# Kernel optimization log

Hardware: AMD Instinct MI355X
Metric: run time of the kernel (lower is better)

The kernel has to match this reference:

```python
import jax, jax.numpy as jnp
import numpy as np

EMBED_DIM = 32
HIDDEN_DIM = 16

def _xavier(key, fan_in, fan_out):
    limit = float(np.sqrt(6.0 / (fan_in + fan_out)))
    return jax.random.uniform(key, (fan_in, fan_out), jnp.float32, -limit, limit)

def setup_inputs() -> dict:
    key = jax.random.key(0)
    ks = jax.random.split(key, 7)
    N = 1_000_000
    H = jax.random.normal(ks[0], (N, EMBED_DIM), jnp.float32)
    TPL = jax.random.normal(ks[1], (1, 1), jnp.float32)
    # params (xavier-uniform weights, zero biases, matching torch init)
    Wv = _xavier(ks[2], EMBED_DIM, HIDDEN_DIM); bv = jnp.zeros((HIDDEN_DIM,), jnp.float32)
    Wu = _xavier(ks[3], EMBED_DIM, HIDDEN_DIM); bu = jnp.zeros((HIDDEN_DIM,), jnp.float32)
    Ww = _xavier(ks[4], HIDDEN_DIM, 1);        bw = jnp.zeros((1,), jnp.float32)
    W1 = _xavier(ks[5], EMBED_DIM + 1, HIDDEN_DIM); b1 = jnp.zeros((HIDDEN_DIM,), jnp.float32)
    W2 = _xavier(ks[6], HIDDEN_DIM, 1);        b2 = jnp.zeros((1,), jnp.float32)
    return {"H": H, "TPL": TPL, "Wv": Wv, "bv": bv, "Wu": Wu, "bu": bu,
            "Ww": Ww, "bw": bw, "W1": W1, "b1": b1, "W2": W2, "b2": b2}

def reference(H, TPL, Wv, bv, Wu, bu, Ww, bw, W1, b1, W2, b2):
    # Gated attention: V (tanh branch) * U (sigmoid branch); dropout off (eval mode)
    V = jnp.tanh(H @ Wv + bv)                       # (N, hid)
    U = jax.nn.sigmoid(H @ Wu + bu)                 # (N, hid)
    G = V * U                                       # (N, hid)
    A_raw = G @ Ww + bw                             # (N, 1)
    alpha = jax.nn.softmax(A_raw.T, axis=1)         # (1, N)
    B = alpha @ H                                   # (1, D) attention-pooled bag rep
    B_fused = jnp.concatenate([B, TPL], axis=1)     # (1, D+1)
    h = jax.nn.relu(B_fused @ W1 + b1)              # (1, hid)
    score = h @ W2 + b2                             # (1, 1)
    return (score, alpha)
```

## Files before the change

kernel.cpp:

```cpp
#include <hip/hip_runtime.h>

#define NBLK   1024
#define TPB    256
#define D      32
#define HID    16
#define CHUNK  16
#define STRIDE 36
#define NWAVES (NBLK * 4)

__global__ __launch_bounds__(TPB, 4)
void k1_logits(const float* __restrict__ H,
               const float* __restrict__ Wv, const float* __restrict__ bv,
               const float* __restrict__ Wu, const float* __restrict__ bu,
               const float* __restrict__ Ww, const float* __restrict__ bw,
               float* __restrict__ eout,
               float* __restrict__ partials,
               int N)
{
    __shared__ float lds[TPB / 64][CHUNK * STRIDE];
    __shared__ float red[TPB / 64][D + 1];

    const int tid  = threadIdx.x;
    const int wave = tid >> 6;
    const int lane = tid & 63;
    const int g    = lane >> 4;
    const int h    = lane & 15;

    float wv[D], wu[D];
    #pragma unroll
    for (int d = 0; d < D; ++d) {
        wv[d] = Wv[d * HID + h];
        wu[d] = Wu[d * HID + h];
    }
    const float bvh = bv[h], buh = bu[h], wwh = Ww[h], bw0 = bw[0];

    float s_acc = 0.0f, vec0 = 0.0f, vec1 = 0.0f;

    float* slice = lds[wave];
    const int nchunk = N / CHUNK;
    int c = blockIdx.x * (TPB / 64) + wave;

    float4 pre0, pre1;
    bool has = (c < nchunk);
    if (has) {
        const float4* src = reinterpret_cast<const float4*>(H + (size_t)c * CHUNK * D);
        pre0 = src[lane];
        pre1 = src[lane + 64];
    }

    while (has) {
        const int cn = c + NWAVES;
        const bool hn = (cn < nchunk);
        float4 nxt0, nxt1;
        if (hn) {
            const float4* src = reinterpret_cast<const float4*>(H + (size_t)cn * CHUNK * D);
            nxt0 = src[lane];
            nxt1 = src[lane + 64];
        }

        {
            const int f0 = lane,      r0i = f0 >> 3, q0 = f0 & 7;
            const int f1 = lane + 64, r1i = f1 >> 3, q1 = f1 & 7;
            *reinterpret_cast<float4*>(&slice[r0i * STRIDE + q0 * 4]) = pre0;
            *reinterpret_cast<float4*>(&slice[r1i * STRIDE + q1 * 4]) = pre1;
        }

        float my_e = 0.0f;
        #pragma unroll
        for (int s = 0; s < 4; ++s) {
            const int rr = s * 4 + g;
            const float* row = &slice[rr * STRIDE];

            float v = bvh, u = buh;
            #pragma unroll
            for (int q = 0; q < 8; ++q) {
                const float4 t4 = *reinterpret_cast<const float4*>(&row[q * 4]);
                v = fmaf(t4.x, wv[q * 4 + 0], v);  u = fmaf(t4.x, wu[q * 4 + 0], u);
                v = fmaf(t4.y, wv[q * 4 + 1], v);  u = fmaf(t4.y, wu[q * 4 + 1], u);
                v = fmaf(t4.z, wv[q * 4 + 2], v);  u = fmaf(t4.z, wu[q * 4 + 2], u);
                v = fmaf(t4.w, wv[q * 4 + 3], v);  u = fmaf(t4.w, wu[q * 4 + 3], u);
            }
            const float th = 1.0f - 2.0f / (__expf(2.0f * v) + 1.0f);
            const float sg = 1.0f / (1.0f + __expf(-u));
            float pa = th * sg * wwh;
            pa += __shfl_xor(pa, 1);
            pa += __shfl_xor(pa, 2);
            pa += __shfl_xor(pa, 4);
            pa += __shfl_xor(pa, 8);
            const float e = __expf(pa + bw0);
            if (h == s) my_e = e;
            s_acc += e;
            const float2 rp = *reinterpret_cast<const float2*>(&row[2 * h]);
            vec0 = fmaf(e, rp.x, vec0);
            vec1 = fmaf(e, rp.y, vec1);
        }
        if (h < 4) eout[c * CHUNK + h * 4 + g] = my_e;

        pre0 = nxt0; pre1 = nxt1;
        c = cn;
        has = hn;
    }

    s_acc += __shfl_xor(s_acc, 16);  s_acc += __shfl_xor(s_acc, 32);
    vec0  += __shfl_xor(vec0, 16);   vec0  += __shfl_xor(vec0, 32);
    vec1  += __shfl_xor(vec1, 16);   vec1  += __shfl_xor(vec1, 32);

    if (lane == 0) red[wave][0] = s_acc;
    if (lane < 16) {
        red[wave][1 + 2 * h] = vec0;
        red[wave][2 + 2 * h] = vec1;
    }
    __syncthreads();
    if (tid < D + 1) {
        float p = red[0][tid] + red[1][tid] + red[2][tid] + red[3][tid];
        partials[(size_t)tid * NBLK + blockIdx.x] = p;
    }
}

__global__ __launch_bounds__(TPB)
void k2a_reduce(const float* __restrict__ partials,
                double* __restrict__ tot,
                float* __restrict__ scalars)
{
    const int j = blockIdx.x, t = threadIdx.x;
    const float4 v = reinterpret_cast<const float4*>(partials + (size_t)j * NBLK)[t];
    double a = (double)v.x + (double)v.y + (double)v.z + (double)v.w;
    #pragma unroll
    for (int m = 1; m <= 32; m <<= 1) a += __shfl_xor(a, m);
    __shared__ double r[TPB / 64];
    if ((t & 63) == 0) r[t >> 6] = a;
    __syncthreads();
    if (t == 0) {
        const double s = r[0] + r[1] + r[2] + r[3];
        tot[j] = s;
        if (j == 0) scalars[0] = (float)(1.0 / s);
    }
}

__global__ __launch_bounds__(TPB)
void k3_alpha(float* __restrict__ alpha,
              const float* __restrict__ scalars,
              const double* __restrict__ tot,
              const float* __restrict__ TPL,
              const float* __restrict__ W1, const float* __restrict__ b1,
              const float* __restrict__ W2, const float* __restrict__ b2,
              float* __restrict__ score_out, int N)
{
    const float invS = scalars[0];
    const int i4 = blockIdx.x * TPB + threadIdx.x;
    const int n4 = (N - 3) >> 2;
    if (i4 < n4) {
        float4* p = reinterpret_cast<float4*>(alpha + 3) + i4;
        float4 v = *p;
        v.x *= invS; v.y *= invS; v.z *= invS; v.w *= invS;
        *p = v;
    } else if (i4 == n4) {
        alpha[0] *= invS; alpha[1] *= invS; alpha[2] *= invS;
        for (int r = 3 + 4 * n4; r < N; ++r) alpha[r] *= invS;
    }
    if (blockIdx.x == 0 && threadIdx.x < HID) {
        const int t = threadIdx.x;
        float hj = b1[t];
        #pragma unroll
        for (int k = 0; k < D; ++k)
            hj = fmaf((float)(tot[1 + k] * (double)invS), W1[k * HID + t], hj);
        hj = fmaf(TPL[0], W1[D * HID + t], hj);
        hj = fmaxf(hj, 0.0f);
        float pre = hj * W2[t];
        pre += __shfl_xor(pre, 1);
        pre += __shfl_xor(pre, 2);
        pre += __shfl_xor(pre, 4);
        pre += __shfl_xor(pre, 8);
        if (t == 0) score_out[0] = pre + b2[0];
    }
}

extern "C" void kernel_launch(void* const* d_in, const int* in_sizes, int n_in,
                              void* d_out, int out_size, void* d_ws, size_t ws_size,
                              hipStream_t stream) {
    const float* H   = (const float*)d_in[0];
    const float* TPL = (const float*)d_in[1];
    const float* Wv  = (const float*)d_in[2];
    const float* bv  = (const float*)d_in[3];
    const float* Wu  = (const float*)d_in[4];
    const float* bu  = (const float*)d_in[5];
    const float* Ww  = (const float*)d_in[6];
    const float* bw  = (const float*)d_in[7];
    const float* W1  = (const float*)d_in[8];
    const float* b1  = (const float*)d_in[9];
    const float* W2  = (const float*)d_in[10];
    const float* b2  = (const float*)d_in[11];

    float* out = (float*)d_out;
    const int N = in_sizes[0] / D;

    float*  ws_f     = (float*)d_ws;
    float*  partials = ws_f;
    double* tot      = (double*)(ws_f + (size_t)(D + 1) * NBLK);
    float*  scalars  = ws_f + (size_t)(D + 1) * NBLK + 2 * (D + 1) + 2;

    k1_logits<<<NBLK, TPB, 0, stream>>>(H, Wv, bv, Wu, bu, Ww, bw,
                                        out + 1, partials, N);
    k2a_reduce<<<D + 1, TPB, 0, stream>>>(partials, tot, scalars);
    const int n4 = (N - 3) >> 2;
    k3_alpha<<<(n4 + 1 + TPB - 1) / TPB, TPB, 0, stream>>>(out + 1, scalars, tot,
                                                           TPL, W1, b1, W2, b2, out, N);
}
```

Baseline: 216.3 us.

## Compute gated-attention projections with bf16 MFMA instead of scalar FMAs

Replaces the per-lane fp32 FMA dot products (staged through LDS) with two 16x16x32 bf16 MFMA instructions per 16-row chunk. Each lane now loads its 8-element slice of a row directly from global memory. Exponentials are shared through a small LDS buffer so that each lane can accumulate the weighted sum for its own H elements. This removes the LDS row staging and most of the ALU work, but it rounds H and the weights to bf16, which loosens accuracy. It also changes the global load pattern and adds an intra-wave LDS exchange.

```diff
diff --git a/kernel.cpp b/kernel.cpp
--- a/kernel.cpp
+++ b/kernel.cpp
@@ -5,8 +5,10 @@
 #define D      32
 #define HID    16
 #define CHUNK  16
-#define STRIDE 36
-#define NWAVES (NBLK * 4)
+#define NWAVES (NBLK * (TPB / 64))
+
+typedef __bf16 bf16x8  __attribute__((ext_vector_type(8)));
+typedef float  floatx4 __attribute__((ext_vector_type(4)));
 
 __global__ __launch_bounds__(TPB, 4)
 void k1_logits(const float* __restrict__ H,
@@ -17,35 +19,39 @@
                float* __restrict__ partials,
                int N)
 {
-    __shared__ float lds[TPB / 64][CHUNK * STRIDE];
+    __shared__ float ldsE[TPB / 64][16];
     __shared__ float red[TPB / 64][D + 1];
 
     const int tid  = threadIdx.x;
     const int wave = tid >> 6;
     const int lane = tid & 63;
-    const int g    = lane >> 4;
-    const int h    = lane & 15;
-
-    float wv[D], wu[D];
-    #pragma unroll
-    for (int d = 0; d < D; ++d) {
-        wv[d] = Wv[d * HID + h];
-        wu[d] = Wu[d * HID + h];
-    }
-    const float bvh = bv[h], buh = bu[h], wwh = Ww[h], bw0 = bw[0];
-
-    float s_acc = 0.0f, vec0 = 0.0f, vec1 = 0.0f;
-
-    float* slice = lds[wave];
+    const int q    = lane >> 4;
+    const int n    = lane & 15;
+
+    bf16x8 bV, bU;
+    #pragma unroll
+    for (int j = 0; j < 8; ++j) {
+        bV[j] = (__bf16)Wv[(q * 8 + j) * HID + n];
+        bU[j] = (__bf16)Wu[(q * 8 + j) * HID + n];
+    }
+    const float bvn = bv[n], bun = bu[n], wwn = Ww[n], bw0 = bw[0];
+
+    float vec[8];
+    #pragma unroll
+    for (int j = 0; j < 8; ++j) vec[j] = 0.0f;
+    float s_acc = 0.0f;
+
     const int nchunk = N / CHUNK;
     int c = blockIdx.x * (TPB / 64) + wave;
+
+    const float* base0 = H + (size_t)n * D + q * 8;
 
     float4 pre0, pre1;
     bool has = (c < nchunk);
     if (has) {
-        const float4* src = reinterpret_cast<const float4*>(H + (size_t)c * CHUNK * D);
-        pre0 = src[lane];
-        pre1 = src[lane + 64];
+        const float* p = base0 + (size_t)c * CHUNK * D;
+        pre0 = *reinterpret_cast<const float4*>(p);
+        pre1 = *reinterpret_cast<const float4*>(p + 4);
     }
 
     while (has) {
@@ -53,62 +59,74 @@
         const bool hn = (cn < nchunk);
         float4 nxt0, nxt1;
         if (hn) {
-            const float4* src = reinterpret_cast<const float4*>(H + (size_t)cn * CHUNK * D);
-            nxt0 = src[lane];
-            nxt1 = src[lane + 64];
+            const float* p = base0 + (size_t)cn * CHUNK * D;
+            nxt0 = *reinterpret_cast<const float4*>(p);
+            nxt1 = *reinterpret_cast<const float4*>(p + 4);
         }
 
-        {
-            const int f0 = lane,      r0i = f0 >> 3, q0 = f0 & 7;
-            const int f1 = lane + 64, r1i = f1 >> 3, q1 = f1 & 7;
-            *reinterpret_cast<float4*>(&slice[r0i * STRIDE + q0 * 4]) = pre0;
-            *reinterpret_cast<float4*>(&slice[r1i * STRIDE + q1 * 4]) = pre1;
-        }
-
-        float my_e = 0.0f;
-        #pragma unroll
-        for (int s = 0; s < 4; ++s) {
-            const int rr = s * 4 + g;
-            const float* row = &slice[rr * STRIDE];
-
-            float v = bvh, u = buh;
-            #pragma unroll
-            for (int q = 0; q < 8; ++q) {
-                const float4 t4 = *reinterpret_cast<const float4*>(&row[q * 4]);
-                v = fmaf(t4.x, wv[q * 4 + 0], v);  u = fmaf(t4.x, wu[q * 4 + 0], u);
-                v = fmaf(t4.y, wv[q * 4 + 1], v);  u = fmaf(t4.y, wu[q * 4 + 1], u);
-                v = fmaf(t4.z, wv[q * 4 + 2], v);  u = fmaf(t4.z, wu[q * 4 + 2], u);
-                v = fmaf(t4.w, wv[q * 4 + 3], v);  u = fmaf(t4.w, wu[q * 4 + 3], u);
-            }
+        bf16x8 a;
+        a[0] = (__bf16)pre0.x; a[1] = (__bf16)pre0.y;
+        a[2] = (__bf16)pre0.z; a[3] = (__bf16)pre0.w;
+        a[4] = (__bf16)pre1.x; a[5] = (__bf16)pre1.y;
+        a[6] = (__bf16)pre1.z; a[7] = (__bf16)pre1.w;
+
+        floatx4 accV = {0.f, 0.f, 0.f, 0.f};
+        floatx4 accU = {0.f, 0.f, 0.f, 0.f};
+        accV = __builtin_amdgcn_mfma_f32_16x16x32_bf16(a, bV, accV, 0, 0, 0);
+        accU = __builtin_amdgcn_mfma_f32_16x16x32_bf16(a, bU, accU, 0, 0, 0);
+
+        float g[4];
+        #pragma unroll
+        for (int r = 0; r < 4; ++r) {
+            const float v  = accV[r] + bvn;
+            const float u  = accU[r] + bun;
             const float th = 1.0f - 2.0f / (__expf(2.0f * v) + 1.0f);
             const float sg = 1.0f / (1.0f + __expf(-u));
-            float pa = th * sg * wwh;
-            pa += __shfl_xor(pa, 1);
-            pa += __shfl_xor(pa, 2);
-            pa += __shfl_xor(pa, 4);
-            pa += __shfl_xor(pa, 8);
-            const float e = __expf(pa + bw0);
-            if (h == s) my_e = e;
-            s_acc += e;
-            const float2 rp = *reinterpret_cast<const float2*>(&row[2 * h]);
-            vec0 = fmaf(e, rp.x, vec0);
-            vec1 = fmaf(e, rp.y, vec1);
+            g[r] = th * sg * wwn;
         }
-        if (h < 4) eout[c * CHUNK + h * 4 + g] = my_e;
+        #pragma unroll
+        for (int r = 0; r < 4; ++r) {
+            g[r] += __shfl_xor(g[r], 1);
+            g[r] += __shfl_xor(g[r], 2);
+            g[r] += __shfl_xor(g[r], 4);
+            g[r] += __shfl_xor(g[r], 8);
+        }
+        float4 e4;
+        e4.x = __expf(g[0] + bw0);
+        e4.y = __expf(g[1] + bw0);
+        e4.z = __expf(g[2] + bw0);
+        e4.w = __expf(g[3] + bw0);
+        if (n == 0) *reinterpret_cast<float4*>(&ldsE[wave][q * 4]) = e4;
+        const float em = ldsE[wave][n];
+        if (lane < 16) eout[(size_t)c * CHUNK + lane] = em;
+        s_acc += em;
+        vec[0] = fmaf(em, pre0.x, vec[0]);
+        vec[1] = fmaf(em, pre0.y, vec[1]);
+        vec[2] = fmaf(em, pre0.z, vec[2]);
+        vec[3] = fmaf(em, pre0.w, vec[3]);
+        vec[4] = fmaf(em, pre1.x, vec[4]);
+        vec[5] = fmaf(em, pre1.y, vec[5]);
+        vec[6] = fmaf(em, pre1.z, vec[6]);
+        vec[7] = fmaf(em, pre1.w, vec[7]);
 
         pre0 = nxt0; pre1 = nxt1;
         c = cn;
         has = hn;
     }
 
-    s_acc += __shfl_xor(s_acc, 16);  s_acc += __shfl_xor(s_acc, 32);
-    vec0  += __shfl_xor(vec0, 16);   vec0  += __shfl_xor(vec0, 32);
-    vec1  += __shfl_xor(vec1, 16);   vec1  += __shfl_xor(vec1, 32);
-
-    if (lane == 0) red[wave][0] = s_acc;
-    if (lane < 16) {
-        red[wave][1 + 2 * h] = vec0;
-        red[wave][2 + 2 * h] = vec1;
+    #pragma unroll
+    for (int m = 1; m <= 32; m <<= 1) s_acc += __shfl_xor(s_acc, m);
+    #pragma unroll
+    for (int j = 0; j < 8; ++j) {
+        vec[j] += __shfl_xor(vec[j], 1);
+        vec[j] += __shfl_xor(vec[j], 2);
+        vec[j] += __shfl_xor(vec[j], 4);
+        vec[j] += __shfl_xor(vec[j], 8);
+    }
+    if (lane == 0) red[wave][0] = 0.25f * s_acc;
+    if (n == 0) {
+        #pragma unroll
+        for (int j = 0; j < 8; ++j) red[wave][1 + q * 8 + j] = vec[j];
     }
     __syncthreads();
     if (tid < D + 1) {
```

New measurement: 211.2 us. -2.4%, faster.
